# Performance work log

Hardware: AMD Instinct MI355X
Metric: run time of the kernel (lower is better)

The kernel has to match this reference:

```python
import jax, jax.numpy as jnp
import numpy as np
import math

NA, D, DA = 8, 512, 64
BSZ, THW = 4, 1024
EPS = 1e-5


def setup_inputs() -> dict:
    key = jax.random.key(0)
    ks = jax.random.split(key, 8)
    x = jax.random.normal(ks[0], (BSZ, THW, D), dtype=jnp.float32)
    B = jax.random.normal(ks[1], (NA, BSZ, THW, THW), dtype=jnp.float32)
    M = jax.random.randint(ks[2], (THW, THW), 0, 2, dtype=jnp.int32)
    # xavier-normal-ish params
    def xavier(k, shape, fan_in, fan_out):
        std = math.sqrt(2.0 / (fan_in + fan_out))
        return jax.random.normal(k, shape, dtype=jnp.float32) * std
    w_q = xavier(ks[3], (NA, D, DA), D, DA)
    w_k = xavier(ks[4], (NA, D, DA), D, DA)
    w_v = xavier(ks[5], (NA, D, DA), D, DA)
    w_proj = xavier(ks[6], (D, NA * DA), NA * DA, D)  # nn.Linear weight [out, in]
    gamma = jnp.ones((D,), dtype=jnp.float32)
    beta = jnp.zeros((D,), dtype=jnp.float32)
    return {"x": x, "B": B, "M": M, "gamma": gamma, "beta": beta,
            "w_q": w_q, "w_k": w_k, "w_v": w_v, "w_proj": w_proj}


def reference(x, B, M, gamma, beta, w_q, w_k, w_v, w_proj):
    b, thw, d = x.shape
    na, _, da = w_q.shape
    # pre-LayerNorm (residual is un-normalized x)
    mu = jnp.mean(x, axis=-1, keepdims=True)
    var = jnp.mean(jnp.square(x - mu), axis=-1, keepdims=True)
    xn = (x - mu) / jnp.sqrt(var + EPS) * gamma + beta  # [b, thw, d]
    # per-head QKV via shared projections: [na, b, thw, da]
    q = jnp.einsum('btd,hde->hbte', xn, w_q)
    k = jnp.einsum('btd,hde->hbte', xn, w_k)
    v = jnp.einsum('btd,hde->hbte', xn, w_v)
    temper = math.sqrt(da)
    attn = jnp.einsum('hbqe,hbke->hbqk', q, k) / temper + B  # [na, b, thw, thw]
    attn = jnp.where(M.astype(bool), jnp.float32(-10000.0), attn)
    p = jax.nn.softmax(attn, axis=-1)
    out = jnp.einsum('hbqk,hbke->hbqe', p, v)  # [na, b, thw, da]
    # concat heads on feature dim: [b, thw, na*da]
    out = out.transpose(1, 2, 0, 3).reshape(b, thw, na * da)
    out = out @ w_proj.T  # [b, thw, d]
    return out + x
```

## Files before the change

kernel.cpp:

```cpp
#include <hip/hip_runtime.h>

typedef __attribute__((ext_vector_type(4))) float f32x4;
typedef __attribute__((ext_vector_type(8))) short bf16x8;

#define AS1 __attribute__((address_space(1)))
#define AS3 __attribute__((address_space(3)))

static __device__ __forceinline__ void gl_lds16(const void* g, void* l) {
  __builtin_amdgcn_global_load_lds((const AS1 unsigned int*)g, (AS3 unsigned int*)l, 16, 0, 0);
}

static __device__ __forceinline__ unsigned short f2bf(float f) {
  union { float f; unsigned u; } v; v.f = f;
  unsigned r = v.u + 0x7FFFu + ((v.u >> 16) & 1u);
  return (unsigned short)(r >> 16);
}

__global__ __launch_bounds__(256) void prep_kernel(
    const float* __restrict__ wq, const float* __restrict__ wk,
    const float* __restrict__ wv, const float* __restrict__ wp,
    const int* __restrict__ M,
    unsigned short* __restrict__ Wt, unsigned short* __restrict__ Wp,
    unsigned* __restrict__ Mbits) {
  const int total = 786432 + 262144 + 32768;
  for (int idx = blockIdx.x * 256 + threadIdx.x; idx < total; idx += gridDim.x * 256) {
    if (idx < 786432) {
      int n = idx >> 9, d = idx & 511;
      int which = n >> 9, h = (n >> 6) & 7, e = n & 63;
      const float* w = (which == 0) ? wq : ((which == 1) ? wk : wv);
      float v = w[h * 32768 + d * 64 + e];
      if (which == 0) v *= 0.125f;
      Wt[idx] = f2bf(v);
    } else if (idx < 786432 + 262144) {
      int i = idx - 786432;
      Wp[i] = f2bf(wp[i]);
    } else {
      int i = idx - 786432 - 262144;
      int r = i >> 5, wd = i & 31;
      const int* row = M + r * 1024 + wd * 32;
      unsigned bits = 0;
#pragma unroll
      for (int b = 0; b < 32; ++b) bits |= (row[b] != 0 ? 1u : 0u) << b;
      Mbits[i] = bits;
    }
  }
}

__global__ __launch_bounds__(256) void ln_kernel(
    const float* __restrict__ x, const float* __restrict__ gamma,
    const float* __restrict__ beta, unsigned short* __restrict__ xn) {
  const int wave = threadIdx.x >> 6, lane = threadIdx.x & 63;
  const int m = blockIdx.x * 4 + wave;
  const float* row = x + (size_t)m * 512;
  float4 a = *(const float4*)(row + lane * 8);
  float4 c = *(const float4*)(row + lane * 8 + 4);
  float s = a.x + a.y + a.z + a.w + c.x + c.y + c.z + c.w;
  float q = a.x * a.x + a.y * a.y + a.z * a.z + a.w * a.w +
            c.x * c.x + c.y * c.y + c.z * c.z + c.w * c.w;
#pragma unroll
  for (int off = 1; off < 64; off <<= 1) {
    s += __shfl_xor(s, off);
    q += __shfl_xor(q, off);
  }
  float mean = s * 0.001953125f;
  float var = q * 0.001953125f - mean * mean;
  float rstd = rsqrtf(var + 1e-5f);
  float4 g0 = *(const float4*)(gamma + lane * 8);
  float4 g1 = *(const float4*)(gamma + lane * 8 + 4);
  float4 b0 = *(const float4*)(beta + lane * 8);
  float4 b1 = *(const float4*)(beta + lane * 8 + 4);
  bf16x8 o;
  o[0] = (short)f2bf((a.x - mean) * rstd * g0.x + b0.x);
  o[1] = (short)f2bf((a.y - mean) * rstd * g0.y + b0.y);
  o[2] = (short)f2bf((a.z - mean) * rstd * g0.z + b0.z);
  o[3] = (short)f2bf((a.w - mean) * rstd * g0.w + b0.w);
  o[4] = (short)f2bf((c.x - mean) * rstd * g1.x + b1.x);
  o[5] = (short)f2bf((c.y - mean) * rstd * g1.y + b1.y);
  o[6] = (short)f2bf((c.z - mean) * rstd * g1.z + b1.z);
  o[7] = (short)f2bf((c.w - mean) * rstd * g1.w + b1.w);
  *(bf16x8*)(xn + (size_t)m * 512 + lane * 8) = o;
}

__global__ __launch_bounds__(256) void gemm_qkv(
    const unsigned short* __restrict__ A, const unsigned short* __restrict__ Bt,
    unsigned short* __restrict__ qout, unsigned short* __restrict__ kout,
    unsigned short* __restrict__ vout) {
  __shared__ __align__(16) unsigned short As[128 * 64];
  __shared__ __align__(16) unsigned short Bs[128 * 64];
  const int bx = blockIdx.x & 31, by = blockIdx.x >> 5;
  const int mbase = bx * 128, nbase = by * 128;
  const int tid = threadIdx.x;
  const int lane = tid & 63, wave = tid >> 6;
  const int lr = lane & 15, lg = lane >> 4;
  const int wm = wave >> 1, wn = wave & 1;
  f32x4 acc[4][4] = {};
  for (int kb = 0; kb < 8; ++kb) {
    const int kbase = kb * 64;
#pragma unroll
    for (int i = 0; i < 4; ++i) {
      int chunk = i * 256 + tid;
      int r = chunk >> 3, kc = chunk & 7;
      gl_lds16(A + (size_t)(mbase + r) * 512 + kbase + kc * 8, &As[chunk * 8]);
    }
#pragma unroll
    for (int i = 0; i < 4; ++i) {
      int chunk = i * 256 + tid;
      int r = chunk >> 3, kc = chunk & 7;
      gl_lds16(Bt + (size_t)(nbase + r) * 512 + kbase + kc * 8, &Bs[chunk * 8]);
    }
    __syncthreads();
#pragma unroll
    for (int ks = 0; ks < 2; ++ks) {
      bf16x8 af[4], bfr[4];
#pragma unroll
      for (int mi = 0; mi < 4; ++mi)
        af[mi] = *(const bf16x8*)&As[(wm * 64 + mi * 16 + lr) * 64 + ks * 32 + lg * 8];
#pragma unroll
      for (int ni = 0; ni < 4; ++ni)
        bfr[ni] = *(const bf16x8*)&Bs[(wn * 64 + ni * 16 + lr) * 64 + ks * 32 + lg * 8];
#pragma unroll
      for (int mi = 0; mi < 4; ++mi)
#pragma unroll
        for (int ni = 0; ni < 4; ++ni)
          acc[mi][ni] = __builtin_amdgcn_mfma_f32_16x16x32_bf16(af[mi], bfr[ni], acc[mi][ni], 0, 0, 0);
    }
    __syncthreads();
  }
#pragma unroll
  for (int ni = 0; ni < 4; ++ni) {
    const int n0 = nbase + wn * 64 + ni * 16;
    const int which = n0 >> 9, h = (n0 >> 6) & 7;
    const int e0 = (n0 & 63) + lr;
    unsigned short* dst = (which == 0) ? qout : ((which == 1) ? kout : vout);
    dst += (size_t)h * 262144 + e0;
#pragma unroll
    for (int mi = 0; mi < 4; ++mi) {
      const int m0 = mbase + wm * 64 + mi * 16 + lg * 4;
#pragma unroll
      for (int j = 0; j < 4; ++j) dst[(size_t)(m0 + j) * 64] = f2bf(acc[mi][ni][j]);
    }
  }
}

__global__ __launch_bounds__(256) void transpose_v(
    const unsigned short* __restrict__ vb, unsigned short* __restrict__ vt) {
  __shared__ unsigned short t[64][72];
  const int h = blockIdx.x >> 6, mt = blockIdx.x & 63;
  const unsigned short* src = vb + (size_t)h * 262144 + (size_t)mt * 64 * 64;
  const int tid = threadIdx.x;
#pragma unroll
  for (int i = 0; i < 2; ++i) {
    int c = tid + 256 * i;
    int r = c >> 3, c8 = c & 7;
    bf16x8 v = *(const bf16x8*)(src + r * 64 + c8 * 8);
#pragma unroll
    for (int k = 0; k < 8; ++k) t[c8 * 8 + k][r] = (unsigned short)v[k];
  }
  __syncthreads();
#pragma unroll
  for (int i = 0; i < 2; ++i) {
    int c = tid + 256 * i;
    int er = c >> 3, mc = c & 7;
    bf16x8 o;
#pragma unroll
    for (int k = 0; k < 8; ++k) o[k] = (short)t[er][mc * 8 + k];
    *(bf16x8*)(vt + (size_t)h * 262144 + (size_t)er * 4096 + mt * 64 + mc * 8) = o;
  }
}

__global__ __launch_bounds__(256) void attn_kernel(
    const unsigned short* __restrict__ qb, const unsigned short* __restrict__ kbuf,
    const unsigned short* __restrict__ vt, const float* __restrict__ Bb,
    const unsigned* __restrict__ Mb, unsigned short* __restrict__ attno) {
  __shared__ __align__(16) unsigned short P[4][16 * 132];
  const int bid = blockIdx.x;
  const int qt = bid & 15, hb = bid >> 4;
  const int h = hb >> 2, b = hb & 3;
  const int lane = threadIdx.x & 63, wave = threadIdx.x >> 6;
  const int lr = lane & 15, lg = lane >> 4;
  const int qa = qt * 64 + wave * 16 + lr;
  const unsigned short* qp = qb + (size_t)h * 262144 + (size_t)(b * 1024 + qa) * 64 + lg * 8;
  const bf16x8 qf0 = *(const bf16x8*)qp;
  const bf16x8 qf1 = *(const bf16x8*)(qp + 32);
  const int qc = qt * 64 + wave * 16 + lg * 4;
  const float* Bp = Bb + (size_t)hb * 1048576;
  float mrun[4] = {-1e30f, -1e30f, -1e30f, -1e30f};
  float lrun[4] = {0.f, 0.f, 0.f, 0.f};
  f32x4 of[4] = {};
  unsigned short* pw = &P[wave][0];
  for (int kv = 0; kv < 8; ++kv) {
    const int kvb = kv * 128;
    float bv[8][4];
    unsigned mwd[4][4];
#pragma unroll
    for (int j = 0; j < 4; ++j) {
      const float* brow = Bp + (size_t)(qc + j) * 1024 + kvb + lr;
#pragma unroll
      for (int f = 0; f < 8; ++f) bv[f][j] = brow[f * 16];
      uint4 mw = *(const uint4*)(Mb + (qc + j) * 32 + (kvb >> 5));
      mwd[j][0] = mw.x; mwd[j][1] = mw.y; mwd[j][2] = mw.z; mwd[j][3] = mw.w;
    }
    f32x4 s[8];
#pragma unroll
    for (int f = 0; f < 8; ++f) {
      const unsigned short* kp =
          kbuf + (size_t)h * 262144 + (size_t)(b * 1024 + kvb + f * 16 + lr) * 64 + lg * 8;
      bf16x8 k0 = *(const bf16x8*)kp;
      bf16x8 k1 = *(const bf16x8*)(kp + 32);
      f32x4 c = {};
      c = __builtin_amdgcn_mfma_f32_16x16x32_bf16(qf0, k0, c, 0, 0, 0);
      c = __builtin_amdgcn_mfma_f32_16x16x32_bf16(qf1, k1, c, 0, 0, 0);
      s[f] = c;
    }
    float scl[4];
#pragma unroll
    for (int j = 0; j < 4; ++j) {
      float mm = -1e30f;
#pragma unroll
      for (int f = 0; f < 8; ++f) {
        float sv = s[f][j] + bv[f][j];
        if ((mwd[j][f >> 1] >> ((f & 1) * 16 + lr)) & 1u) sv = -10000.f;
        s[f][j] = sv;
        mm = fmaxf(mm, sv);
      }
      mm = fmaxf(mm, __shfl_xor(mm, 1));
      mm = fmaxf(mm, __shfl_xor(mm, 2));
      mm = fmaxf(mm, __shfl_xor(mm, 4));
      mm = fmaxf(mm, __shfl_xor(mm, 8));
      float mn = fmaxf(mrun[j], mm);
      scl[j] = __expf(mrun[j] - mn);
      mrun[j] = mn;
      float ps = 0.f;
#pragma unroll
      for (int f = 0; f < 8; ++f) {
        float p = __expf(s[f][j] - mn);
        s[f][j] = p;
        ps += p;
      }
      ps += __shfl_xor(ps, 1);
      ps += __shfl_xor(ps, 2);
      ps += __shfl_xor(ps, 4);
      ps += __shfl_xor(ps, 8);
      lrun[j] = lrun[j] * scl[j] + ps;
    }
#pragma unroll
    for (int e = 0; e < 4; ++e) {
      of[e][0] *= scl[0]; of[e][1] *= scl[1]; of[e][2] *= scl[2]; of[e][3] *= scl[3];
    }
#pragma unroll
    for (int f = 0; f < 8; ++f)
#pragma unroll
      for (int j = 0; j < 4; ++j)
        pw[(lg * 4 + j) * 132 + f * 16 + lr] = f2bf(s[f][j]);
    __syncthreads();
    bf16x8 pa[4];
#pragma unroll
    for (int ks = 0; ks < 4; ++ks)
      pa[ks] = *(const bf16x8*)&pw[lr * 132 + ks * 32 + lg * 8];
#pragma unroll
    for (int e = 0; e < 4; ++e) {
      const unsigned short* vp =
          vt + (size_t)h * 262144 + (size_t)(e * 16 + lr) * 4096 + b * 1024 + kvb + lg * 8;
#pragma unroll
      for (int ks = 0; ks < 4; ++ks) {
        bf16x8 vf = *(const bf16x8*)(vp + ks * 32);
        of[e] = __builtin_amdgcn_mfma_f32_16x16x32_bf16(pa[ks], vf, of[e], 0, 0, 0);
      }
    }
    __syncthreads();
  }
#pragma unroll
  for (int e = 0; e < 4; ++e)
#pragma unroll
    for (int j = 0; j < 4; ++j) {
      int m = b * 1024 + qc + j;
      attno[(size_t)h * 262144 + (size_t)m * 64 + e * 16 + lr] = f2bf(of[e][j] / lrun[j]);
    }
}

__global__ __launch_bounds__(256) void gemm_proj(
    const unsigned short* __restrict__ attno, const unsigned short* __restrict__ Wp,
    const float* __restrict__ x, float* __restrict__ out) {
  __shared__ __align__(16) unsigned short As[128 * 64];
  __shared__ __align__(16) unsigned short Bs[128 * 64];
  const int bx = blockIdx.x & 31, by = blockIdx.x >> 5;
  const int mbase = bx * 128, nbase = by * 128;
  const int tid = threadIdx.x;
  const int lane = tid & 63, wave = tid >> 6;
  const int lr = lane & 15, lg = lane >> 4;
  const int wm = wave >> 1, wn = wave & 1;
  f32x4 acc[4][4] = {};
  for (int kb = 0; kb < 8; ++kb) {
#pragma unroll
    for (int i = 0; i < 4; ++i) {
      int chunk = i * 256 + tid;
      int r = chunk >> 3, kc = chunk & 7;
      gl_lds16(attno + (size_t)kb * 262144 + (size_t)(mbase + r) * 64 + kc * 8, &As[chunk * 8]);
    }
#pragma unroll
    for (int i = 0; i < 4; ++i) {
      int chunk = i * 256 + tid;
      int r = chunk >> 3, kc = chunk & 7;
      gl_lds16(Wp + (size_t)(nbase + r) * 512 + kb * 64 + kc * 8, &Bs[chunk * 8]);
    }
    __syncthreads();
#pragma unroll
    for (int ks = 0; ks < 2; ++ks) {
      bf16x8 af[4], bfr[4];
#pragma unroll
      for (int mi = 0; mi < 4; ++mi)
        af[mi] = *(const bf16x8*)&As[(wm * 64 + mi * 16 + lr) * 64 + ks * 32 + lg * 8];
#pragma unroll
      for (int ni = 0; ni < 4; ++ni)
        bfr[ni] = *(const bf16x8*)&Bs[(wn * 64 + ni * 16 + lr) * 64 + ks * 32 + lg * 8];
#pragma unroll
      for (int mi = 0; mi < 4; ++mi)
#pragma unroll
        for (int ni = 0; ni < 4; ++ni)
          acc[mi][ni] = __builtin_amdgcn_mfma_f32_16x16x32_bf16(af[mi], bfr[ni], acc[mi][ni], 0, 0, 0);
    }
    __syncthreads();
  }
#pragma unroll
  for (int ni = 0; ni < 4; ++ni) {
    const int n = nbase + wn * 64 + ni * 16 + lr;
#pragma unroll
    for (int mi = 0; mi < 4; ++mi) {
      const int m0 = mbase + wm * 64 + mi * 16 + lg * 4;
#pragma unroll
      for (int j = 0; j < 4; ++j) {
        size_t idx = (size_t)(m0 + j) * 512 + n;
        out[idx] = acc[mi][ni][j] + x[idx];
      }
    }
  }
}

extern "C" void kernel_launch(void* const* d_in, const int* in_sizes, int n_in,
                              void* d_out, int out_size, void* d_ws, size_t ws_size,
                              hipStream_t stream) {
  const float* x = (const float*)d_in[0];
  const float* B = (const float*)d_in[1];
  const int* M = (const int*)d_in[2];
  const float* gamma = (const float*)d_in[3];
  const float* beta = (const float*)d_in[4];
  const float* wq = (const float*)d_in[5];
  const float* wk = (const float*)d_in[6];
  const float* wv = (const float*)d_in[7];
  const float* wp = (const float*)d_in[8];
  float* out = (float*)d_out;

  char* ws = (char*)d_ws;
  size_t o = 0;
  auto alloc = [&](size_t bytes) {
    void* p = ws + o;
    o += (bytes + 255) & ~(size_t)255;
    return p;
  };
  unsigned short* xn    = (unsigned short*)alloc(4096ull * 512 * 2);
  unsigned short* Wt    = (unsigned short*)alloc(1536ull * 512 * 2);
  unsigned short* Wp    = (unsigned short*)alloc(512ull * 512 * 2);
  unsigned*       Mb    = (unsigned*)alloc(1024ull * 32 * 4);
  unsigned short* qb    = (unsigned short*)alloc(8ull * 4096 * 64 * 2);
  unsigned short* kb    = (unsigned short*)alloc(8ull * 4096 * 64 * 2);
  unsigned short* vb    = (unsigned short*)alloc(8ull * 4096 * 64 * 2);
  unsigned short* vt    = (unsigned short*)alloc(8ull * 64 * 4096 * 2);
  unsigned short* attno = (unsigned short*)alloc(8ull * 4096 * 64 * 2);
  (void)ws_size; (void)in_sizes; (void)n_in; (void)out_size;

  hipLaunchKernelGGL(prep_kernel, dim3(2048), dim3(256), 0, stream,
                     wq, wk, wv, wp, M, Wt, Wp, Mb);
  hipLaunchKernelGGL(ln_kernel, dim3(1024), dim3(256), 0, stream, x, gamma, beta, xn);
  hipLaunchKernelGGL(gemm_qkv, dim3(384), dim3(256), 0, stream, xn, Wt, qb, kb, vb);
  hipLaunchKernelGGL(transpose_v, dim3(512), dim3(256), 0, stream, vb, vt);
  hipLaunchKernelGGL(attn_kernel, dim3(512), dim3(256), 0, stream, qb, kb, vt, B, Mb, attno);
  hipLaunchKernelGGL(gemm_proj, dim3(128), dim3(256), 0, stream, attno, Wp, x, out);
}
```

Measured before the change: 294.8 us.

## Vectorize prep kernel, remap attention blocks per XCD, and halve proj GEMM tiles

The prep kernel is rewritten so weight transposes go through an LDS tile with vectorized float4 loads and bf16x8 stores, and the mask bit-packing uses int4 loads. The attention kernel now maps blocks so all query tiles of one head/batch land on the same XCD, which should improve L2 reuse of K/V. It also hoists K and V fragment loads ahead of the MFMAs, drops the two per-iteration barriers (each wave only touches its own P slice), and adds a two-blocks-per-CU occupancy hint. The projection GEMM uses 128x64 tiles to double the grid to 256 blocks for better CU coverage, at the cost of re-reading the A tiles more often.

```diff
diff --git a/kernel.cpp b/kernel.cpp
--- a/kernel.cpp
+++ b/kernel.cpp
@@ -22,29 +22,60 @@
     const int* __restrict__ M,
     unsigned short* __restrict__ Wt, unsigned short* __restrict__ Wp,
     unsigned* __restrict__ Mbits) {
-  const int total = 786432 + 262144 + 32768;
-  for (int idx = blockIdx.x * 256 + threadIdx.x; idx < total; idx += gridDim.x * 256) {
-    if (idx < 786432) {
-      int n = idx >> 9, d = idx & 511;
-      int which = n >> 9, h = (n >> 6) & 7, e = n & 63;
-      const float* w = (which == 0) ? wq : ((which == 1) ? wk : wv);
-      float v = w[h * 32768 + d * 64 + e];
-      if (which == 0) v *= 0.125f;
-      Wt[idx] = f2bf(v);
-    } else if (idx < 786432 + 262144) {
-      int i = idx - 786432;
-      Wp[i] = f2bf(wp[i]);
-    } else {
-      int i = idx - 786432 - 262144;
-      int r = i >> 5, wd = i & 31;
-      const int* row = M + r * 1024 + wd * 32;
-      unsigned bits = 0;
-#pragma unroll
-      for (int b = 0; b < 32; ++b) bits |= (row[b] != 0 ? 1u : 0u) << b;
-      Mbits[i] = bits;
-    }
-  }
-}
+  const int blk = blockIdx.x, tid = threadIdx.x;
+  if (blk < 192) {
+    __shared__ unsigned short t[64][72];
+    const int which = blk >> 6, rem = blk & 63;
+    const int h = rem >> 3, dt = rem & 7, d0 = dt * 64;
+    const float* w = (which == 0) ? wq : ((which == 1) ? wk : wv);
+    const float scale = (which == 0) ? 0.125f : 1.0f;
+    const int r = tid >> 2, c4 = tid & 3;
+    const float* src = w + h * 32768 + (d0 + r) * 64 + c4 * 16;
+#pragma unroll
+    for (int i = 0; i < 4; ++i) {
+      float4 v = *(const float4*)(src + i * 4);
+      t[c4 * 16 + i * 4 + 0][r] = f2bf(v.x * scale);
+      t[c4 * 16 + i * 4 + 1][r] = f2bf(v.y * scale);
+      t[c4 * 16 + i * 4 + 2][r] = f2bf(v.z * scale);
+      t[c4 * 16 + i * 4 + 3][r] = f2bf(v.w * scale);
+    }
+    __syncthreads();
+    const int e = tid >> 2;
+    const int n = which * 512 + h * 64 + e;
+    unsigned short* dst = Wt + (size_t)n * 512 + d0 + c4 * 16;
+#pragma unroll
+    for (int i = 0; i < 2; ++i) {
+      bf16x8 o;
+#pragma unroll
+      for (int k = 0; k < 8; ++k) o[k] = (short)t[e][c4 * 16 + i * 8 + k];
+      *(bf16x8*)(dst + i * 8) = o;
+    }
+  } else if (blk < 320) {
+    const int base = ((blk - 192) * 256 + tid) * 8;
+    float4 a = *(const float4*)(wp + base);
+    float4 c = *(const float4*)(wp + base + 4);
+    bf16x8 o;
+    o[0] = (short)f2bf(a.x); o[1] = (short)f2bf(a.y);
+    o[2] = (short)f2bf(a.z); o[3] = (short)f2bf(a.w);
+    o[4] = (short)f2bf(c.x); o[5] = (short)f2bf(c.y);
+    o[6] = (short)f2bf(c.z); o[7] = (short)f2bf(c.w);
+    *(bf16x8*)(Wp + base) = o;
+  } else {
+    const int wi = (blk - 320) * 256 + tid;
+    const int* row = M + wi * 32;
+    unsigned bits = 0;
+#pragma unroll
+    for (int i = 0; i < 8; ++i) {
+      int4 v = *(const int4*)(row + i * 4);
+      bits |= (v.x != 0 ? 1u : 0u) << (i * 4 + 0);
+      bits |= (v.y != 0 ? 1u : 0u) << (i * 4 + 1);
+      bits |= (v.z != 0 ? 1u : 0u) << (i * 4 + 2);
+      bits |= (v.w != 0 ? 1u : 0u) << (i * 4 + 3);
+    }
+    Mbits[wi] = bits;
+  }
+}
+
 
 __global__ __launch_bounds__(256) void ln_kernel(
     const float* __restrict__ x, const float* __restrict__ gamma,
@@ -168,20 +199,24 @@
   }
 }
 
-__global__ __launch_bounds__(256) void attn_kernel(
+__global__ __launch_bounds__(256, 2) void attn_kernel(
     const unsigned short* __restrict__ qb, const unsigned short* __restrict__ kbuf,
     const unsigned short* __restrict__ vt, const float* __restrict__ Bb,
     const unsigned* __restrict__ Mb, unsigned short* __restrict__ attno) {
   __shared__ __align__(16) unsigned short P[4][16 * 132];
-  const int bid = blockIdx.x;
-  const int qt = bid & 15, hb = bid >> 4;
+  const int g = blockIdx.x;
+  const int xcd = g & 7, slot = g >> 3;
+  const int hb = xcd + 8 * (slot >> 4);
+  const int qt = slot & 15;
   const int h = hb >> 2, b = hb & 3;
   const int lane = threadIdx.x & 63, wave = threadIdx.x >> 6;
   const int lr = lane & 15, lg = lane >> 4;
+  const unsigned short* qh = qb + (size_t)h * 262144 + (size_t)b * 65536;
+  const unsigned short* kh = kbuf + (size_t)h * 262144 + (size_t)b * 65536;
+  const unsigned short* vh = vt + (size_t)h * 262144 + b * 1024;
   const int qa = qt * 64 + wave * 16 + lr;
-  const unsigned short* qp = qb + (size_t)h * 262144 + (size_t)(b * 1024 + qa) * 64 + lg * 8;
-  const bf16x8 qf0 = *(const bf16x8*)qp;
-  const bf16x8 qf1 = *(const bf16x8*)(qp + 32);
+  const bf16x8 qf0 = *(const bf16x8*)(qh + (size_t)qa * 64 + lg * 8);
+  const bf16x8 qf1 = *(const bf16x8*)(qh + (size_t)qa * 64 + lg * 8 + 32);
   const int qc = qt * 64 + wave * 16 + lg * 4;
   const float* Bp = Bb + (size_t)hb * 1048576;
   float mrun[4] = {-1e30f, -1e30f, -1e30f, -1e30f};
@@ -197,19 +232,22 @@
       const float* brow = Bp + (size_t)(qc + j) * 1024 + kvb + lr;
 #pragma unroll
       for (int f = 0; f < 8; ++f) bv[f][j] = brow[f * 16];
-      uint4 mw = *(const uint4*)(Mb + (qc + j) * 32 + (kvb >> 5));
+      uint4 mw = *(const uint4*)(Mb + (qc + j) * 32 + kv * 4);
       mwd[j][0] = mw.x; mwd[j][1] = mw.y; mwd[j][2] = mw.z; mwd[j][3] = mw.w;
     }
+    bf16x8 kf0[8], kf1[8];
+#pragma unroll
+    for (int f = 0; f < 8; ++f) {
+      const unsigned short* kp = kh + (size_t)(kvb + f * 16 + lr) * 64 + lg * 8;
+      kf0[f] = *(const bf16x8*)kp;
+      kf1[f] = *(const bf16x8*)(kp + 32);
+    }
     f32x4 s[8];
 #pragma unroll
     for (int f = 0; f < 8; ++f) {
-      const unsigned short* kp =
-          kbuf + (size_t)h * 262144 + (size_t)(b * 1024 + kvb + f * 16 + lr) * 64 + lg * 8;
-      bf16x8 k0 = *(const bf16x8*)kp;
-      bf16x8 k1 = *(const bf16x8*)(kp + 32);
       f32x4 c = {};
-      c = __builtin_amdgcn_mfma_f32_16x16x32_bf16(qf0, k0, c, 0, 0, 0);
-      c = __builtin_amdgcn_mfma_f32_16x16x32_bf16(qf1, k1, c, 0, 0, 0);
+      c = __builtin_amdgcn_mfma_f32_16x16x32_bf16(qf0, kf0[f], c, 0, 0, 0);
+      c = __builtin_amdgcn_mfma_f32_16x16x32_bf16(qf1, kf1[f], c, 0, 0, 0);
       s[f] = c;
     }
     float scl[4];
@@ -252,22 +290,22 @@
 #pragma unroll
       for (int j = 0; j < 4; ++j)
         pw[(lg * 4 + j) * 132 + f * 16 + lr] = f2bf(s[f][j]);
-    __syncthreads();
     bf16x8 pa[4];
 #pragma unroll
     for (int ks = 0; ks < 4; ++ks)
       pa[ks] = *(const bf16x8*)&pw[lr * 132 + ks * 32 + lg * 8];
+    bf16x8 vf[4][4];
 #pragma unroll
     for (int e = 0; e < 4; ++e) {
-      const unsigned short* vp =
-          vt + (size_t)h * 262144 + (size_t)(e * 16 + lr) * 4096 + b * 1024 + kvb + lg * 8;
-#pragma unroll
-      for (int ks = 0; ks < 4; ++ks) {
-        bf16x8 vf = *(const bf16x8*)(vp + ks * 32);
-        of[e] = __builtin_amdgcn_mfma_f32_16x16x32_bf16(pa[ks], vf, of[e], 0, 0, 0);
-      }
-    }
-    __syncthreads();
+      const unsigned short* vp = vh + (size_t)(e * 16 + lr) * 4096 + kvb + lg * 8;
+#pragma unroll
+      for (int ks = 0; ks < 4; ++ks) vf[e][ks] = *(const bf16x8*)(vp + ks * 32);
+    }
+#pragma unroll
+    for (int e = 0; e < 4; ++e)
+#pragma unroll
+      for (int ks = 0; ks < 4; ++ks)
+        of[e] = __builtin_amdgcn_mfma_f32_16x16x32_bf16(pa[ks], vf[e][ks], of[e], 0, 0, 0);
   }
 #pragma unroll
   for (int e = 0; e < 4; ++e)
@@ -282,14 +320,14 @@
     const unsigned short* __restrict__ attno, const unsigned short* __restrict__ Wp,
     const float* __restrict__ x, float* __restrict__ out) {
   __shared__ __align__(16) unsigned short As[128 * 64];
-  __shared__ __align__(16) unsigned short Bs[128 * 64];
+  __shared__ __align__(16) unsigned short Bs[64 * 64];
   const int bx = blockIdx.x & 31, by = blockIdx.x >> 5;
-  const int mbase = bx * 128, nbase = by * 128;
+  const int mbase = bx * 128, nbase = by * 64;
   const int tid = threadIdx.x;
   const int lane = tid & 63, wave = tid >> 6;
   const int lr = lane & 15, lg = lane >> 4;
   const int wm = wave >> 1, wn = wave & 1;
-  f32x4 acc[4][4] = {};
+  f32x4 acc[4][2] = {};
   for (int kb = 0; kb < 8; ++kb) {
 #pragma unroll
     for (int i = 0; i < 4; ++i) {
@@ -298,7 +336,7 @@
       gl_lds16(attno + (size_t)kb * 262144 + (size_t)(mbase + r) * 64 + kc * 8, &As[chunk * 8]);
     }
 #pragma unroll
-    for (int i = 0; i < 4; ++i) {
+    for (int i = 0; i < 2; ++i) {
       int chunk = i * 256 + tid;
       int r = chunk >> 3, kc = chunk & 7;
       gl_lds16(Wp + (size_t)(nbase + r) * 512 + kb * 64 + kc * 8, &Bs[chunk * 8]);
@@ -306,24 +344,24 @@
     __syncthreads();
 #pragma unroll
     for (int ks = 0; ks < 2; ++ks) {
-      bf16x8 af[4], bfr[4];
+      bf16x8 af[4], bfr[2];
 #pragma unroll
       for (int mi = 0; mi < 4; ++mi)
         af[mi] = *(const bf16x8*)&As[(wm * 64 + mi * 16 + lr) * 64 + ks * 32 + lg * 8];
 #pragma unroll
-      for (int ni = 0; ni < 4; ++ni)
-        bfr[ni] = *(const bf16x8*)&Bs[(wn * 64 + ni * 16 + lr) * 64 + ks * 32 + lg * 8];
+      for (int ni = 0; ni < 2; ++ni)
+        bfr[ni] = *(const bf16x8*)&Bs[(wn * 32 + ni * 16 + lr) * 64 + ks * 32 + lg * 8];
 #pragma unroll
       for (int mi = 0; mi < 4; ++mi)
 #pragma unroll
-        for (int ni = 0; ni < 4; ++ni)
+        for (int ni = 0; ni < 2; ++ni)
           acc[mi][ni] = __builtin_amdgcn_mfma_f32_16x16x32_bf16(af[mi], bfr[ni], acc[mi][ni], 0, 0, 0);
     }
     __syncthreads();
   }
 #pragma unroll
-  for (int ni = 0; ni < 4; ++ni) {
-    const int n = nbase + wn * 64 + ni * 16 + lr;
+  for (int ni = 0; ni < 2; ++ni) {
+    const int n = nbase + wn * 32 + ni * 16 + lr;
 #pragma unroll
     for (int mi = 0; mi < 4; ++mi) {
       const int m0 = mbase + wm * 64 + mi * 16 + lg * 4;
@@ -368,11 +406,11 @@
   unsigned short* attno = (unsigned short*)alloc(8ull * 4096 * 64 * 2);
   (void)ws_size; (void)in_sizes; (void)n_in; (void)out_size;
 
-  hipLaunchKernelGGL(prep_kernel, dim3(2048), dim3(256), 0, stream,
+  hipLaunchKernelGGL(prep_kernel, dim3(448), dim3(256), 0, stream,
                      wq, wk, wv, wp, M, Wt, Wp, Mb);
   hipLaunchKernelGGL(ln_kernel, dim3(1024), dim3(256), 0, stream, x, gamma, beta, xn);
   hipLaunchKernelGGL(gemm_qkv, dim3(384), dim3(256), 0, stream, xn, Wt, qb, kb, vb);
   hipLaunchKernelGGL(transpose_v, dim3(512), dim3(256), 0, stream, vb, vt);
   hipLaunchKernelGGL(attn_kernel, dim3(512), dim3(256), 0, stream, qb, kb, vt, B, Mb, attno);
-  hipLaunchKernelGGL(gemm_proj, dim3(128), dim3(256), 0, stream, attno, Wp, x, out);
-}
+  hipLaunchKernelGGL(gemm_proj, dim3(256), dim3(256), 0, stream, attno, Wp, x, out);
+}
```

After: 293.5 us. About the same (-0.5%).
